# Kernel tuning notes

Hardware: AMD Instinct MI355X
Metric: run time of the kernel (lower is better)

## Reference

```python
import jax, jax.numpy as jnp
import numpy as np

N = 50000   # nodes
E = 800000  # edges
G = 64      # graphs
NEG_SLOPE = 0.2  # PyG GATConv leaky_relu slope


def gat_conv(x, edge_index, edge_attr, W, att_src, att_dst, We, att_edge, bias, num_nodes):
    # PyG GATConv, add_self_loops=False, concat=True, eval (no dropout)
    H, C = att_src.shape
    h = (x @ W).reshape(-1, H, C)                      # [N,H,C]
    a_src = (h * att_src).sum(-1)                      # [N,H]
    a_dst = (h * att_dst).sum(-1)                      # [N,H]
    src, dst = edge_index[0], edge_index[1]
    e = (edge_attr @ We).reshape(-1, H, C)             # [E,H,C]
    a_edge = (e * att_edge).sum(-1)                    # [E,H]
    alpha = a_src[src] + a_dst[dst] + a_edge           # [E,H]
    alpha = jax.nn.leaky_relu(alpha, NEG_SLOPE)
    # segment softmax over incoming edges of each dst node
    amax = jax.ops.segment_max(alpha, dst, num_segments=num_nodes)
    amax = jnp.where(jnp.isfinite(amax), amax, 0.0)
    ex = jnp.exp(alpha - amax[dst])
    denom = jax.ops.segment_sum(ex, dst, num_segments=num_nodes)
    att = ex / (denom[dst] + 1e-16)                    # [E,H]
    msg = h[src] * att[..., None]                      # [E,H,C]
    out = jax.ops.segment_sum(msg, dst, num_segments=num_nodes)
    return out.reshape(num_nodes, H * C) + bias


def setup_inputs() -> dict:
    key = jax.random.key(0)
    ks = jax.random.split(key, 20)
    s = 0.1
    inp = {
        "x": jax.random.normal(ks[0], (N, 128), jnp.float32),
        "edge_index": jax.random.randint(ks[1], (2, E), 0, N, dtype=jnp.int32),
        "edge_attr": jax.random.normal(ks[2], (E, 1), jnp.float32),
        "batch": jnp.sort(jax.random.randint(ks[3], (N,), 0, G, dtype=jnp.int32)),
        # layer 1: 128 -> 4 heads x 32
        "W1": jax.random.normal(ks[4], (128, 128), jnp.float32) * s,
        "as1": jax.random.normal(ks[5], (4, 32), jnp.float32) * s,
        "ad1": jax.random.normal(ks[6], (4, 32), jnp.float32) * s,
        "We1": jax.random.normal(ks[7], (1, 128), jnp.float32) * s,
        "ae1": jax.random.normal(ks[8], (4, 32), jnp.float32) * s,
        "b1": jnp.zeros((128,), jnp.float32),
        # layer 2: 128 -> 1 head x 64
        "W2": jax.random.normal(ks[9], (128, 64), jnp.float32) * s,
        "as2": jax.random.normal(ks[10], (1, 64), jnp.float32) * s,
        "ad2": jax.random.normal(ks[11], (1, 64), jnp.float32) * s,
        "We2": jax.random.normal(ks[12], (1, 64), jnp.float32) * s,
        "ae2": jax.random.normal(ks[13], (1, 64), jnp.float32) * s,
        "b2": jnp.zeros((64,), jnp.float32),
        # prediction head
        "Wp": jax.random.normal(ks[14], (64, 1), jnp.float32) * s,
        "bp": jnp.zeros((1,), jnp.float32),
    }
    return inp


def reference(x, edge_index, edge_attr, batch, W1, as1, ad1, We1, ae1, b1,
              W2, as2, ad2, We2, ae2, b2, Wp, bp):
    h = gat_conv(x, edge_index, edge_attr, W1, as1, ad1, We1, ae1, b1, N)
    h = jax.nn.relu(h)  # dropout p=0.0, eval mode
    h = gat_conv(h, edge_index, edge_attr, W2, as2, ad2, We2, ae2, b2, N)
    # per-graph mean pooling (vectorized replacement of the python loop)
    counts = jax.ops.segment_sum(jnp.ones((N,), h.dtype), batch, num_segments=G)
    sums = jax.ops.segment_sum(h, batch, num_segments=G)   # [G,64]
    mean = sums / counts[:, None]
    out = mean @ Wp + bp                                   # [G,1]
    return out.squeeze(-1)                                 # [G]
```

## Files before the change

### kernel.cpp

```cpp
#include <hip/hip_runtime.h>
#include <hip/hip_bf16.h>

typedef unsigned short u16;
typedef unsigned int u32;

#define MAXB 2048
#define POOL_MAXG 64

typedef __attribute__((ext_vector_type(8))) short bf16x8;
typedef __attribute__((ext_vector_type(4))) float f32x4;

__device__ __forceinline__ float bf2f(u16 u) { return __uint_as_float(((u32)u) << 16); }
__device__ __forceinline__ float bl(u32 u) { return __uint_as_float(u << 16); }
__device__ __forceinline__ float bh(u32 u) { return __uint_as_float(u & 0xffff0000u); }
__device__ __forceinline__ u16 f2bf(float f) {
    u32 u = __float_as_uint(f);
    u += 0x7fffu + ((u >> 16) & 1u);
    return (u16)(u >> 16);
}
__device__ __forceinline__ float lrelu(float x) { return x > 0.f ? x : 0.2f * x; }
__device__ __forceinline__ int clampi(int v, int lo, int hi) {
    return v < lo ? lo : (v > hi ? hi : v);
}
__device__ __forceinline__ float load1(const void* base, int idx, int f32) {
    return f32 ? ((const float*)base)[idx] : bf2f(((const u16*)base)[idx]);
}
__device__ __forceinline__ float cexpf(float a) {
    return __builtin_amdgcn_exp2f(fminf(a, 30.f) * 1.4426950408889634f);
}

__global__ void k_init(const u32* __restrict__ xw, int* __restrict__ flag,
                       int* __restrict__ bcnt, int B,
                       const void* We1, const void* ae1, const void* We2, const void* ae2,
                       const void* as1, const void* ad1, const void* as2, const void* ad2,
                       float* __restrict__ consts, float* __restrict__ pool, int psize) {
    __shared__ int sf;
    int t = threadIdx.x;
    for (int i = t; i < B; i += 256) bcnt[i] = 0;
    if (t < 64) {
        int cnt = 0;
        #pragma unroll
        for (int j = 0; j < 4; j++) {
            u32 w = xw[t * 4 + j];
            int e0 = (int)((w >> 7) & 0xffu);
            int e1 = (int)((w >> 23) & 0xffu);
            cnt += (e0 >= 0x60 && e0 <= 0x8f);
            cnt += (e1 >= 0x60 && e1 <= 0x8f);
        }
        #pragma unroll
        for (int off = 32; off > 0; off >>= 1) cnt += __shfl_xor(cnt, off);
        if (t == 0) { int v = (cnt < 480) ? 1 : 0; *flag = v; sf = v; }
    }
    __syncthreads();
    int f = sf;
    for (int i = t; i < psize; i += 256) pool[i] = 0.f;
    if (t < 4) {
        float s = 0.f;
        for (int c = 0; c < 32; c++) s += load1(We1, t * 32 + c, f) * load1(ae1, t * 32 + c, f);
        consts[t] = s;
    } else if (t == 4) {
        float s = 0.f;
        for (int c = 0; c < 64; c++) s += load1(We2, c, f) * load1(ae2, c, f);
        consts[4] = s;
    }
    if (t < 128) {
        consts[8 + t] = load1(as1, t, f);
        consts[136 + t] = load1(ad1, t, f);
    }
    if (t < 64) {
        consts[264 + t] = load1(as2, t, f);
        consts[328 + t] = load1(ad2, t, f);
    }
}

template <int NC>
__global__ __launch_bounds__(256, 2) void k_gemm_mfma(
    const void* __restrict__ X, const void* __restrict__ Wg,
    const int* __restrict__ flag, int fXovr, u16* __restrict__ Y,
    const float* __restrict__ consts, float* __restrict__ casrc,
    float* __restrict__ cadst, int nrows) {
    constexpr int NCT = NC / 16;
    __shared__ __align__(16) u16 Bf[2][NCT][4][64][8];

    const int f = *flag;
    const bool fX = (fXovr < 0) ? (f != 0) : (fXovr != 0);
    const bool fW = (f != 0);
    const int tid = threadIdx.x;
    const int wid = tid >> 6, lane = tid & 63;

    if (fW) {
        const float* W4 = (const float*)Wg;
        for (int g = tid; g < 128 * NC / 4; g += 256) {
            int e = g * 4;
            int r = e / NC;
            int c = e % NC;
            int k = (NC == 64) ? ((r < 64) ? 2 * r : 2 * (r - 64) + 1) : r;
            int s = k >> 5;
            int kk = k & 31;
            int lhi = (kk >> 3) << 4;
            int j = kk & 7;
            float4 v = *(const float4*)(W4 + e);
            float vv[4] = {v.x, v.y, v.z, v.w};
            #pragma unroll
            for (int q = 0; q < 4; q++) {
                int col = c + q;
                int t = col >> 4, l = lhi | (col & 15);
                u16 h = f2bf(vv[q]);
                Bf[0][t][s][l][j] = h;
                Bf[1][t][s][l][j] = f2bf(vv[q] - bf2f(h));
            }
        }
    } else {
        const u16* Wb = (const u16*)Wg;
        for (int g = tid; g < 128 * NC / 8; g += 256) {
            int e = g * 8;
            int r = e / NC;
            int c = e % NC;
            int k = (NC == 64) ? ((r < 64) ? 2 * r : 2 * (r - 64) + 1) : r;
            int s = k >> 5;
            int kk = k & 31;
            int lhi = (kk >> 3) << 4;
            int j = kk & 7;
            uint4 v = *(const uint4*)(Wb + e);
            u16 arr[8] = {(u16)v.x, (u16)(v.x >> 16), (u16)v.y, (u16)(v.y >> 16),
                          (u16)v.z, (u16)(v.z >> 16), (u16)v.w, (u16)(v.w >> 16)};
            #pragma unroll
            for (int q = 0; q < 8; q++) {
                int col = c + q;
                int t = col >> 4, l = lhi | (col & 15);
                Bf[0][t][s][l][j] = arr[q];
            }
        }
    }
    __syncthreads();

    const int tileIds[2] = {(int)blockIdx.x, (int)(blockIdx.x + gridDim.x)};

    bf16x8 ahi[2][4], alo[2][4];
    #pragma unroll
    for (int tt = 0; tt < 2; tt++) {
        const int rowbase = tileIds[tt] * 64 + wid * 16;
        const int arow = rowbase + (lane & 15);
        const bool rv = arow < nrows;
        #pragma unroll
        for (int s = 0; s < 4; s++) {
            int koff = s * 32 + (lane >> 4) * 8;
            u16 h[8], l8[8];
            #pragma unroll
            for (int j = 0; j < 8; j++) { h[j] = 0; l8[j] = 0; }
            if (rv) {
                if (fX) {
                    const float* xp = (const float*)X + (size_t)arow * 128 + koff;
                    float4 a = *(const float4*)xp;
                    float4 b = *(const float4*)(xp + 4);
                    float vv[8];
                    vv[0] = a.x; vv[1] = a.y; vv[2] = a.z; vv[3] = a.w;
                    vv[4] = b.x; vv[5] = b.y; vv[6] = b.z; vv[7] = b.w;
                    #pragma unroll
                    for (int j = 0; j < 8; j++) {
                        h[j] = f2bf(vv[j]);
                        l8[j] = f2bf(vv[j] - bf2f(h[j]));
                    }
                } else {
                    const u16* xp = (const u16*)X + (size_t)arow * 128 + koff;
                    uint4 q = *(const uint4*)xp;
                    h[0] = (u16)q.x; h[1] = (u16)(q.x >> 16);
                    h[2] = (u16)q.y; h[3] = (u16)(q.y >> 16);
                    h[4] = (u16)q.z; h[5] = (u16)(q.z >> 16);
                    h[6] = (u16)q.w; h[7] = (u16)(q.w >> 16);
                }
            }
            bf16x8 vh, vl;
            #pragma unroll
            for (int j = 0; j < 8; j++) { vh[j] = (short)h[j]; vl[j] = (short)l8[j]; }
            ahi[tt][s] = vh; alo[tt][s] = vl;
        }
    }

    f32x4 acc[2][NCT];
    #pragma unroll
    for (int tt = 0; tt < 2; tt++)
        #pragma unroll
        for (int t = 0; t < NCT; t++) acc[tt][t] = (f32x4){0.f, 0.f, 0.f, 0.f};
    #pragma unroll
    for (int s = 0; s < 4; s++) {
        #pragma unroll
        for (int t = 0; t < NCT; t++) {
            bf16x8 bhi = *(const bf16x8*)&Bf[0][t][s][lane][0];
            acc[0][t] = __builtin_amdgcn_mfma_f32_16x16x32_bf16(ahi[0][s], bhi, acc[0][t], 0, 0, 0);
            acc[1][t] = __builtin_amdgcn_mfma_f32_16x16x32_bf16(ahi[1][s], bhi, acc[1][t], 0, 0, 0);
            if (fW) {
                bf16x8 blo = *(const bf16x8*)&Bf[1][t][s][lane][0];
                acc[0][t] = __builtin_amdgcn_mfma_f32_16x16x32_bf16(ahi[0][s], blo, acc[0][t], 0, 0, 0);
                acc[1][t] = __builtin_amdgcn_mfma_f32_16x16x32_bf16(ahi[1][s], blo, acc[1][t], 0, 0, 0);
            }
            if (fX) {
                acc[0][t] = __builtin_amdgcn_mfma_f32_16x16x32_bf16(alo[0][s], bhi, acc[0][t], 0, 0, 0);
                acc[1][t] = __builtin_amdgcn_mfma_f32_16x16x32_bf16(alo[1][s], bhi, acc[1][t], 0, 0, 0);
            }
        }
    }

    #pragma unroll
    for (int tt = 0; tt < 2; tt++) {
        const int rowbase = tileIds[tt] * 64 + wid * 16;
        const int l16 = lane & 15;
        #pragma unroll
        for (int reg = 0; reg < 4; reg++) {
            int r = rowbase + (lane >> 4) * 4 + reg;
            if (r < nrows) {
                if constexpr (NC == 128) {
                    #pragma unroll
                    for (int t = 0; t < 4; t++) {
                        u32 w = (u32)f2bf(acc[tt][t][reg])
                              | ((u32)f2bf(acc[tt][t + 4][reg]) << 16);
                        ((u32*)Y)[(size_t)r * 64 + t * 16 + l16] = w;
                    }
                } else {
                    #pragma unroll
                    for (int t = 0; t < 4; t++)
                        Y[(size_t)r * 64 + t * 16 + l16] = f2bf(acc[tt][t][reg]);
                }
            }
        }
        if (casrc) {
            if constexpr (NC == 128) {
                #pragma unroll
                for (int reg = 0; reg < 4; reg++) {
                    int r = rowbase + (lane >> 4) * 4 + reg;
                    float pA[4] = {0.f, 0.f, 0.f, 0.f};
                    float pD[4] = {0.f, 0.f, 0.f, 0.f};
                    #pragma unroll
                    for (int t = 0; t < 4; t++) {
                        int p = t * 16 + l16;
                        int g = t >> 1;
                        pA[g]     += acc[tt][t][reg]     * consts[8 + p];
                        pD[g]     += acc[tt][t][reg]     * consts[136 + p];
                        pA[g + 2] += acc[tt][t + 4][reg] * consts[72 + p];
                        pD[g + 2] += acc[tt][t + 4][reg] * consts[200 + p];
                    }
                    #pragma unroll
                    for (int off = 1; off < 16; off <<= 1) {
                        #pragma unroll
                        for (int g = 0; g < 4; g++) {
                            pA[g] += __shfl_xor(pA[g], off);
                            pD[g] += __shfl_xor(pD[g], off);
                        }
                    }
                    if (l16 == 0 && r < nrows) {
                        #pragma unroll
                        for (int g = 0; g < 4; g++) {
                            casrc[r * 4 + g] = pA[g];
                            cadst[r * 4 + g] = pD[g];
                        }
                    }
                }
            } else {
                #pragma unroll
                for (int reg = 0; reg < 4; reg++) {
                    int r = rowbase + (lane >> 4) * 4 + reg;
                    float s1 = 0.f, s2 = 0.f;
                    #pragma unroll
                    for (int t = 0; t < 4; t++) {
                        int p = t * 16 + l16;
                        s1 += acc[tt][t][reg] * consts[264 + p];
                        s2 += acc[tt][t][reg] * consts[328 + p];
                    }
                    #pragma unroll
                    for (int off = 1; off < 16; off <<= 1) {
                        s1 += __shfl_xor(s1, off);
                        s2 += __shfl_xor(s2, off);
                    }
                    if (l16 == 0 && r < nrows) { casrc[r] = s1; cadst[r] = s2; }
                }
            }
        }
    }
}

__global__ __launch_bounds__(256) void k_bhist2(const int* __restrict__ dst,
                                                int* __restrict__ bcnt, int E, int n, int B) {
    __shared__ int lh[MAXB];
    for (int i = threadIdx.x; i < B; i += 256) lh[i] = 0;
    __syncthreads();
    int stride = gridDim.x * 256;
    for (int e = blockIdx.x * 256 + threadIdx.x; e < E; e += stride) {
        int d = clampi(dst[e], 0, n - 1);
        atomicAdd(&lh[d >> 8], 1);
    }
    __syncthreads();
    for (int i = threadIdx.x; i < B; i += 256)
        if (lh[i]) atomicAdd(&bcnt[i], lh[i]);
}
__global__ void k_bscan(const int* __restrict__ bcnt, int* __restrict__ bbase,
                        int* __restrict__ bfront, int* __restrict__ roff,
                        int B, int N, int E) {
    __shared__ int buf[256];
    __shared__ int carry;
    int t = threadIdx.x;
    if (t == 0) carry = 0;
    __syncthreads();
    for (int base = 0; base < B; base += 256) {
        int k = base + t;
        int v = (k < B) ? bcnt[k] : 0;
        buf[t] = v;
        __syncthreads();
        for (int off = 1; off < 256; off <<= 1) {
            int u = (t >= off) ? buf[t - off] : 0;
            __syncthreads();
            buf[t] += u;
            __syncthreads();
        }
        int excl = carry + buf[t] - v;
        if (k < B) { bbase[k] = excl; bfront[k] = excl; }
        __syncthreads();
        if (t == 0) carry += buf[255];
        __syncthreads();
    }
    if (t == 0) { bbase[B] = carry; roff[N] = E; }
}
__global__ void k_zero(int* __restrict__ p, int n) {
    int i = blockIdx.x * 256 + threadIdx.x;
    if (i < n) p[i] = 0;
}
__global__ __launch_bounds__(256) void k_bhist(const int* __restrict__ dst,
                                               int* __restrict__ cnt, int* __restrict__ bcnt,
                                               int E, int n, int B) {
    __shared__ int lh[MAXB];
    for (int i = threadIdx.x; i < B; i += 256) lh[i] = 0;
    __syncthreads();
    int stride = gridDim.x * 256;
    for (int e = blockIdx.x * 256 + threadIdx.x; e < E; e += stride) {
        int d = clampi(dst[e], 0, n - 1);
        atomicAdd(&cnt[d], 1);
        atomicAdd(&lh[d >> 8], 1);
    }
    __syncthreads();
    for (int i = threadIdx.x; i < B; i += 256)
        if (lh[i]) atomicAdd(&bcnt[i], lh[i]);
}
__global__ void k_scan1(const int* __restrict__ cnt, int* __restrict__ part,
                        int* __restrict__ bsum, int n) {
    __shared__ int buf[256];
    int i = blockIdx.x * 256 + threadIdx.x;
    int v = (i < n) ? cnt[i] : 0;
    buf[threadIdx.x] = v;
    __syncthreads();
    for (int off = 1; off < 256; off <<= 1) {
        int t = (threadIdx.x >= off) ? buf[threadIdx.x - off] : 0;
        __syncthreads();
        buf[threadIdx.x] += t;
        __syncthreads();
    }
    if (i < n) part[i] = buf[threadIdx.x];
    if (threadIdx.x == 255) bsum[blockIdx.x] = buf[255];
}
__global__ void k_scan3b(int* __restrict__ roff, const int* __restrict__ bsum,
                         int* __restrict__ rpos, int n, int nb) {
    __shared__ int buf[256];
    int t = threadIdx.x;
    int v = (t < nb) ? bsum[t] : 0;
    buf[t] = v;
    __syncthreads();
    for (int off = 1; off < 256; off <<= 1) {
        int u = (t >= off) ? buf[t - off] : 0;
        __syncthreads();
        buf[t] += u;
        __syncthreads();
    }
    __shared__ int excl[256];
    excl[t] = buf[t] - v;
    __syncthreads();
    int i = blockIdx.x * 256 + t;
    if (i > n) return;
    int val;
    if (i == 0) { val = 0; roff[0] = 0; }
    else { val = roff[i] + excl[(i - 1) >> 8]; roff[i] = val; }
    if (i < n) rpos[i] = val;
}
__global__ __launch_bounds__(256) void k_binA(
    const int* __restrict__ dst, const int* __restrict__ src, const void* eattr,
    const int* __restrict__ flag, int* __restrict__ bfront, int2* __restrict__ stagedA,
    int E, int n, int B) {
    __shared__ int lhist[MAXB];
    __shared__ int lbase[MAXB];
    int f = *flag;
    constexpr int T = 2048;
    for (int tile = blockIdx.x; (long long)tile * T < E; tile += gridDim.x) {
        int base = tile * T;
        for (int i = threadIdx.x; i < B; i += 256) lhist[i] = 0;
        __syncthreads();
        int sj0, sj1, sj2, sj3, sj4, sj5, sj6, sj7;
        int dj0, dj1, dj2, dj3, dj4, dj5, dj6, dj7;
        int rj0, rj1, rj2, rj3, rj4, rj5, rj6, rj7;
        int ej0, ej1, ej2, ej3, ej4, ej5, ej6, ej7;
        #define BINA_LOAD(J, SJ, DJ, RJ, EJ)                                   \
        {                                                                      \
            int idx = base + (J) * 256 + threadIdx.x;                          \
            bool v = idx < E;                                                  \
            int d = v ? clampi(dst[idx], 0, n - 1) : 0;                        \
            SJ = v ? clampi(src[idx], 0, n - 1) : 0;                           \
            EJ = v ? __float_as_int(load1(eattr, idx, f)) : 0;                 \
            DJ = d;                                                            \
            RJ = v ? atomicAdd(&lhist[d >> 8], 1) : -1;                        \
        }
        BINA_LOAD(0, sj0, dj0, rj0, ej0)
        BINA_LOAD(1, sj1, dj1, rj1, ej1)
        BINA_LOAD(2, sj2, dj2, rj2, ej2)
        BINA_LOAD(3, sj3, dj3, rj3, ej3)
        BINA_LOAD(4, sj4, dj4, rj4, ej4)
        BINA_LOAD(5, sj5, dj5, rj5, ej5)
        BINA_LOAD(6, sj6, dj6, rj6, ej6)
        BINA_LOAD(7, sj7, dj7, rj7, ej7)
        #undef BINA_LOAD
        __syncthreads();
        for (int i = threadIdx.x; i < B; i += 256) {
            int c = lhist[i];
            lbase[i] = c ? atomicAdd(&bfront[i], c) : 0;
        }
        __syncthreads();
        #define BINA_STORE(SJ, DJ, RJ, EJ)                                     \
        if (RJ >= 0) {                                                         \
            long long q = (long long)lbase[DJ >> 8] + RJ;                      \
            if (q >= 0 && q < E) {                                             \
                int2 v2;                                                       \
                v2.x = (SJ & 0xFFFFFF) | ((DJ & 255) << 24);                   \
                v2.y = EJ;                                                     \
                stagedA[q] = v2;                                               \
            }                                                                  \
        }
        BINA_STORE(sj0, dj0, rj0, ej0)
        BINA_STORE(sj1, dj1, rj1, ej1)
        BINA_STORE(sj2, dj2, rj2, ej2)
        BINA_STORE(sj3, dj3, rj3, ej3)
        BINA_STORE(sj4, dj4, rj4, ej4)
        BINA_STORE(sj5, dj5, rj5, ej5)
        BINA_STORE(sj6, dj6, rj6, ej6)
        BINA_STORE(sj7, dj7, rj7, ej7)
        #undef BINA_STORE
        __syncthreads();
    }
}
__global__ __launch_bounds__(256) void k_binB2(
    const int2* __restrict__ stagedA, const int* __restrict__ bbase,
    int* __restrict__ roff, int2* __restrict__ edata, int N, int E, int B) {
    __shared__ int lcnt[256];
    __shared__ int buf[256];
    __shared__ int lpos[256];
    int k = blockIdx.x;
    int t = threadIdx.x;
    lcnt[t] = 0;
    __syncthreads();
    int lo = clampi(bbase[k], 0, E);
    int hi = clampi(bbase[k + 1], lo, E);
    for (int i = lo + t; i < hi; i += 256)
        atomicAdd(&lcnt[(stagedA[i].x >> 24) & 255], 1);
    __syncthreads();
    int v = lcnt[t];
    buf[t] = v;
    __syncthreads();
    for (int off = 1; off < 256; off <<= 1) {
        int u = (t >= off) ? buf[t - off] : 0;
        __syncthreads();
        buf[t] += u;
        __syncthreads();
    }
    int pos = lo + buf[t] - v;
    int dn = (k << 8) + t;
    if (dn < N) roff[dn] = pos;
    lpos[t] = pos;
    __syncthreads();
    for (int i = lo + t; i < hi; i += 256) {
        int2 a = stagedA[i];
        int p = atomicAdd(&lpos[(a.x >> 24) & 255], 1);
        if (p >= 0 && p < E) edata[p] = make_int2(a.x & 0xFFFFFF, a.y);
    }
}
__global__ void k_scatter(const int* __restrict__ dst, const int* __restrict__ src,
                          const void* eattr, const int* __restrict__ flag,
                          int* __restrict__ rpos, int2* __restrict__ edata, int E, int n) {
    int f = *flag;
    int e = blockIdx.x * 256 + threadIdx.x;
    if (e < E) {
        int d = clampi(dst[e], 0, n - 1);
        int s = clampi(src[e], 0, n - 1);
        float ea = load1(eattr, e, f);
        int p = atomicAdd(&rpos[d], 1);
        if (p >= 0 && p < E) {
            int2 v; v.x = s; v.y = __float_as_int(ea);
            edata[p] = v;
        }
    }
}

__global__ __launch_bounds__(256) void k_gat1c(
    const u32* __restrict__ hp, const float* __restrict__ asrc, const float* __restrict__ adst,
    const int2* __restrict__ edata, const int* __restrict__ roff,
    const int* __restrict__ flag, const float* __restrict__ consts, const void* bias,
    u32* __restrict__ out, int n, int E) {
    __shared__ float4 wls[4][64];
    int f = *flag;
    int gtid = blockIdx.x * 256 + threadIdx.x;
    int wv = gtid >> 6, lane = gtid & 63;
    int wid = (threadIdx.x >> 6);
    int nw = (gridDim.x * 256) >> 6;
    const float c0 = consts[0], c1 = consts[1], c2 = consts[2], c3 = consts[3];
    const int hl = lane & 31;
    const int sel = lane >> 5;
    const int p0 = hl * 2;
    const int phsel = hl >> 4;
    const float biasA0 = load1(bias, p0, f);
    const float biasB0 = load1(bias, 64 + p0, f);
    const float biasA1 = load1(bias, p0 + 1, f);
    const float biasB1 = load1(bias, 64 + p0 + 1, f);
    const int ghsel = lane >> 5;
    const float gbiasA = load1(bias, lane, f);
    const float gbiasB = load1(bias, 64 + lane, f);

    for (int db = wv * 2; db < n; db += nw * 2) {
        int d = db + sel;
        bool dv = d < n;
        int dcl = dv ? d : 0;
        int s0 = dv ? clampi(roff[d], 0, E) : 0;
        int s1 = dv ? clampi(roff[d + 1], s0, E) : 0;
        int deg = s1 - s0;

        if (__all(deg <= 32)) {
            float4 adv = *(const float4*)&adst[(size_t)dcl * 4];
            bool v = hl < deg;
            int s = 0;
            float e0 = 0.f, e1 = 0.f, e2 = 0.f, e3 = 0.f;
            if (v) {
                int2 ed = edata[s0 + hl];
                s = ed.x;
                float ea = __int_as_float(ed.y);
                float4 av = *(const float4*)&asrc[(size_t)s * 4];
                e0 = cexpf(lrelu(av.x + adv.x + ea * c0));
                e1 = cexpf(lrelu(av.y + adv.y + ea * c1));
                e2 = cexpf(lrelu(av.z + adv.z + ea * c2));
                e3 = cexpf(lrelu(av.w + adv.w + ea * c3));
            }
            float d0 = e0, d1 = e1, d2 = e2, d3 = e3;
            #pragma unroll
            for (int off = 16; off > 0; off >>= 1) {
                d0 += __shfl_xor(d0, off); d1 += __shfl_xor(d1, off);
                d2 += __shfl_xor(d2, off); d3 += __shfl_xor(d3, off);
            }
            float i0 = 1.f / (d0 + 1e-16f), i1 = 1.f / (d1 + 1e-16f);
            float i2 = 1.f / (d2 + 1e-16f), i3 = 1.f / (d3 + 1e-16f);
            wls[wid][lane] = make_float4(e0 * i0, e1 * i1, e2 * i2, e3 * i3);

            int degm = max(deg, __shfl_xor(deg, 32));
            int base = sel * 32;
            float aA0 = 0.f, aB0 = 0.f, aA1 = 0.f, aB1 = 0.f;
            for (int j = 0; j < degm; j += 4) {
                int j0 = base + j, j1 = base + j + 1, j2 = base + j + 2, j3 = base + j + 3;
                int sa = __shfl(s, j0), sb = __shfl(s, j1);
                int sc_ = __shfl(s, j2), sd = __shfl(s, j3);
                float4 wa = wls[wid][j0], wb = wls[wid][j1];
                float4 wc = wls[wid][j2], wd = wls[wid][j3];
                uint2 ha = *(const uint2*)(hp + (size_t)sa * 64 + p0);
                uint2 hb = *(const uint2*)(hp + (size_t)sb * 64 + p0);
                uint2 hc = *(const uint2*)(hp + (size_t)sc_ * 64 + p0);
                uint2 hd = *(const uint2*)(hp + (size_t)sd * 64 + p0);
                float wAa = phsel ? wa.y : wa.x, wBa = phsel ? wa.w : wa.z;
                float wAb = phsel ? wb.y : wb.x, wBb = phsel ? wb.w : wb.z;
                float wAc = phsel ? wc.y : wc.x, wBc = phsel ? wc.w : wc.z;
                float wAd = phsel ? wd.y : wd.x, wBd = phsel ? wd.w : wd.z;
                aA0 += wAa * bl(ha.x); aB0 += wBa * bh(ha.x);
                aA1 += wAa * bl(ha.y); aB1 += wBa * bh(ha.y);
                aA0 += wAb * bl(hb.x); aB0 += wBb * bh(hb.x);
                aA1 += wAb * bl(hb.y); aB1 += wBb * bh(hb.y);
                aA0 += wAc * bl(hc.x); aB0 += wBc * bh(hc.x);
                aA1 += wAc * bl(hc.y); aB1 += wBc * bh(hc.y);
                aA0 += wAd * bl(hd.x); aB0 += wBd * bh(hd.x);
                aA1 += wAd * bl(hd.y); aB1 += wBd * bh(hd.y);
            }
            if (dv) {
                u32 w0 = (u32)f2bf(fmaxf(aA0 + biasA0, 0.f))
                       | ((u32)f2bf(fmaxf(aB0 + biasB0, 0.f)) << 16);
                u32 w1 = (u32)f2bf(fmaxf(aA1 + biasA1, 0.f))
                       | ((u32)f2bf(fmaxf(aB1 + biasB1, 0.f)) << 16);
                *(uint2*)(out + (size_t)d * 64 + p0) = make_uint2(w0, w1);
            }
        } else {
            for (int q = 0; q < 2; q++) {
                int dq = db + q;
                if (dq >= n) break;
                int t0 = clampi(roff[dq], 0, E);
                int t1 = clampi(roff[dq + 1], t0, E);
                int dg = t1 - t0;
                float4 adv = *(const float4*)&adst[(size_t)dq * 4];
                if (dg <= 64) {
                    bool v = lane < dg;
                    int s = 0;
                    float e0 = 0.f, e1 = 0.f, e2 = 0.f, e3 = 0.f;
                    if (v) {
                        int2 ed = edata[t0 + lane];
                        s = ed.x;
                        float ea = __int_as_float(ed.y);
                        float4 av = *(const float4*)&asrc[(size_t)s * 4];
                        e0 = cexpf(lrelu(av.x + adv.x + ea * c0));
                        e1 = cexpf(lrelu(av.y + adv.y + ea * c1));
                        e2 = cexpf(lrelu(av.z + adv.z + ea * c2));
                        e3 = cexpf(lrelu(av.w + adv.w + ea * c3));
                    }
                    float d0 = e0, d1 = e1, d2 = e2, d3 = e3;
                    #pragma unroll
                    for (int off = 32; off > 0; off >>= 1) {
                        d0 += __shfl_xor(d0, off); d1 += __shfl_xor(d1, off);
                        d2 += __shfl_xor(d2, off); d3 += __shfl_xor(d3, off);
                    }
                    float i0 = 1.f / (d0 + 1e-16f), i1 = 1.f / (d1 + 1e-16f);
                    float i2 = 1.f / (d2 + 1e-16f), i3 = 1.f / (d3 + 1e-16f);
                    wls[wid][lane] = make_float4(e0 * i0, e1 * i1, e2 * i2, e3 * i3);

                    float aA0 = 0.f, aB0 = 0.f, aA1 = 0.f, aB1 = 0.f;
                    for (int j = 0; j < dg; j += 4) {
                        int j0 = j + sel, j1 = j + 2 + sel;
                        int sa = __shfl(s, j0), sb = __shfl(s, j1);
                        float4 wa = wls[wid][j0], wb = wls[wid][j1];
                        uint2 ha = *(const uint2*)(hp + (size_t)sa * 64 + p0);
                        uint2 hb = *(const uint2*)(hp + (size_t)sb * 64 + p0);
                        float wAa = phsel ? wa.y : wa.x, wBa = phsel ? wa.w : wa.z;
                        float wAb = phsel ? wb.y : wb.x, wBb = phsel ? wb.w : wb.z;
                        aA0 += wAa * bl(ha.x); aB0 += wBa * bh(ha.x);
                        aA1 += wAa * bl(ha.y); aB1 += wBa * bh(ha.y);
                        aA0 += wAb * bl(hb.x); aB0 += wBb * bh(hb.x);
                        aA1 += wAb * bl(hb.y); aB1 += wBb * bh(hb.y);
                    }
                    aA0 += __shfl_xor(aA0, 32); aB0 += __shfl_xor(aB0, 32);
                    aA1 += __shfl_xor(aA1, 32); aB1 += __shfl_xor(aB1, 32);
                    if (lane < 32) {
                        u32 w0 = (u32)f2bf(fmaxf(aA0 + biasA0, 0.f))
                               | ((u32)f2bf(fmaxf(aB0 + biasB0, 0.f)) << 16);
                        u32 w1 = (u32)f2bf(fmaxf(aA1 + biasA1, 0.f))
                               | ((u32)f2bf(fmaxf(aB1 + biasB1, 0.f)) << 16);
                        *(uint2*)(out + (size_t)dq * 64 + p0) = make_uint2(w0, w1);
                    }
                } else {
                    float d0 = 0.f, d1 = 0.f, d2 = 0.f, d3 = 0.f;
                    for (int idx = t0 + lane; idx < t1; idx += 64) {
                        int2 ed = edata[idx];
                        float ea = __int_as_float(ed.y);
                        float4 av = *(const float4*)&asrc[(size_t)ed.x * 4];
                        d0 += cexpf(lrelu(av.x + adv.x + ea * c0));
                        d1 += cexpf(lrelu(av.y + adv.y + ea * c1));
                        d2 += cexpf(lrelu(av.z + adv.z + ea * c2));
                        d3 += cexpf(lrelu(av.w + adv.w + ea * c3));
                    }
                    #pragma unroll
                    for (int off = 32; off > 0; off >>= 1) {
                        d0 += __shfl_xor(d0, off); d1 += __shfl_xor(d1, off);
                        d2 += __shfl_xor(d2, off); d3 += __shfl_xor(d3, off);
                    }
                    float i0 = 1.f / (d0 + 1e-16f), i1 = 1.f / (d1 + 1e-16f);
                    float i2 = 1.f / (d2 + 1e-16f), i3 = 1.f / (d3 + 1e-16f);
                    float iA = ghsel ? i1 : i0, iB = ghsel ? i3 : i2;
                    float cA = ghsel ? c1 : c0, cB = ghsel ? c3 : c2;
                    float aA = ghsel ? adv.y : adv.x, aB = ghsel ? adv.w : adv.z;
                    float accA = 0.f, accB = 0.f;
                    for (int idx = t0; idx < t1; idx++) {
                        int2 ed = edata[idx];
                        float ea = __int_as_float(ed.y);
                        float4 av = *(const float4*)&asrc[(size_t)ed.x * 4];
                        float wA = cexpf(lrelu((ghsel ? av.y : av.x) + aA + ea * cA)) * iA;
                        float wB = cexpf(lrelu((ghsel ? av.w : av.z) + aB + ea * cB)) * iB;
                        u32 hw = hp[(size_t)ed.x * 64 + lane];
                        accA += wA * bl(hw);
                        accB += wB * bh(hw);
                    }
                    float rA = fmaxf(accA + gbiasA, 0.f);
                    float rB = fmaxf(accB + gbiasB, 0.f);
                    out[(size_t)dq * 64 + lane] = (u32)f2bf(rA) | ((u32)f2bf(rB) << 16);
                }
            }
        }
    }
}

__global__ __launch_bounds__(256) void k_gat2c(
    const u16* __restrict__ h, const float* __restrict__ asrc, const float* __restrict__ adst,
    const int2* __restrict__ edata, const int* __restrict__ roff,
    const int* __restrict__ flag, const float* __restrict__ consts, const void* bias,
    u16* __restrict__ out, int n, int E) {
    __shared__ float wls[4][64];
    int f = *flag;
    int gtid = blockIdx.x * 256 + threadIdx.x;
    int wv = gtid >> 6, lane = gtid & 63;
    int wid = (threadIdx.x >> 6);
    int nw = (gridDim.x * 256) >> 6;
    const float C = consts[4];
    const int hl = lane & 31;
    const int sel = lane >> 5;
    const int p0 = hl * 2;
    const float bias0 = load1(bias, p0, f);
    const float bias1 = load1(bias, p0 + 1, f);
    const float gbias = load1(bias, lane, f);

    for (int db = wv * 2; db < n; db += nw * 2) {
        int d = db + sel;
        bool dv = d < n;
        int s0 = dv ? clampi(roff[d], 0, E) : 0;
        int s1 = dv ? clampi(roff[d + 1], s0, E) : 0;
        int deg = s1 - s0;
        float ad = dv ? adst[d] : 0.f;

        if (__all(deg <= 32)) {
            bool v = hl < deg;
            int s = 0;
            float e = 0.f;
            if (v) {
                int2 ed = edata[s0 + hl];
                s = ed.x;
                e = cexpf(lrelu(asrc[s] + ad + __int_as_float(ed.y) * C));
            }
            float den = e;
            #pragma unroll
            for (int off = 16; off > 0; off >>= 1) den += __shfl_xor(den, off);
            float inv = 1.f / (den + 1e-16f);
            wls[wid][lane] = e * inv;

            int degm = max(deg, __shfl_xor(deg, 32));
            int base = sel * 32;
            float a0 = 0.f, a1 = 0.f;
            for (int j = 0; j < degm; j += 4) {
                int j0 = base + j, j1 = base + j + 1, j2 = base + j + 2, j3 = base + j + 3;
                int sa = __shfl(s, j0), sb = __shfl(s, j1);
                int sc_ = __shfl(s, j2), sd = __shfl(s, j3);
                float wa = wls[wid][j0], wb = wls[wid][j1];
                float wc = wls[wid][j2], wd = wls[wid][j3];
                u32 ha = *(const u32*)(h + (size_t)sa * 64 + p0);
                u32 hb = *(const u32*)(h + (size_t)sb * 64 + p0);
                u32 hc = *(const u32*)(h + (size_t)sc_ * 64 + p0);
                u32 hd = *(const u32*)(h + (size_t)sd * 64 + p0);
                a0 += wa * bl(ha) + wb * bl(hb) + wc * bl(hc) + wd * bl(hd);
                a1 += wa * bh(ha) + wb * bh(hb) + wc * bh(hc) + wd * bh(hd);
            }
            if (dv) {
                u32 w = (u32)f2bf(a0 + bias0) | ((u32)f2bf(a1 + bias1) << 16);
                *(u32*)(out + (size_t)d * 64 + p0) = w;
            }
        } else {
            for (int q = 0; q < 2; q++) {
                int dq = db + q;
                if (dq >= n) break;
                int t0 = clampi(roff[dq], 0, E);
                int t1 = clampi(roff[dq + 1], t0, E);
                int dg = t1 - t0;
                float adq = adst[dq];
                if (dg <= 64) {
                    bool v = lane < dg;
                    int s = 0;
                    float e = 0.f;
                    if (v) {
                        int2 ed = edata[t0 + lane];
                        s = ed.x;
                        e = cexpf(lrelu(asrc[s] + adq + __int_as_float(ed.y) * C));
                    }
                    float den = e;
                    #pragma unroll
                    for (int off = 32; off > 0; off >>= 1) den += __shfl_xor(den, off);
                    float inv = 1.f / (den + 1e-16f);
                    wls[wid][lane] = e * inv;

                    float a0 = 0.f, a1 = 0.f;
                    for (int j = 0; j < dg; j += 4) {
                        int j0 = j + sel, j1 = j + 2 + sel;
                        int sa = __shfl(s, j0), sb = __shfl(s, j1);
                        float wa = wls[wid][j0], wb = wls[wid][j1];
                        u32 ha = *(const u32*)(h + (size_t)sa * 64 + p0);
                        u32 hb = *(const u32*)(h + (size_t)sb * 64 + p0);
                        a0 += wa * bl(ha) + wb * bl(hb);
                        a1 += wa * bh(ha) + wb * bh(hb);
                    }
                    a0 += __shfl_xor(a0, 32);
                    a1 += __shfl_xor(a1, 32);
                    if (lane < 32) {
                        u32 w = (u32)f2bf(a0 + bias0) | ((u32)f2bf(a1 + bias1) << 16);
                        *(u32*)(out + (size_t)dq * 64 + p0) = w;
                    }
                } else {
                    float den = 0.f;
                    for (int idx = t0 + lane; idx < t1; idx += 64) {
                        int2 ed = edata[idx];
                        den += cexpf(lrelu(asrc[ed.x] + adq + __int_as_float(ed.y) * C));
                    }
                    #pragma unroll
                    for (int off = 32; off > 0; off >>= 1) den += __shfl_xor(den, off);
                    float inv = 1.f / (den + 1e-16f);
                    float acc = 0.f;
                    for (int idx = t0; idx < t1; idx++) {
                        int2 ed = edata[idx];
                        float w = cexpf(lrelu(asrc[ed.x] + adq
                                              + __int_as_float(ed.y) * C)) * inv;
                        acc += w * bf2f(h[(size_t)ed.x * 64 + lane]);
                    }
                    out[(size_t)dq * 64 + lane] = f2bf(acc + gbias);
                }
            }
        }
    }
}

__global__ __launch_bounds__(256) void k_gat1f(
    const u32* __restrict__ hp, const float* __restrict__ asrc, const float* __restrict__ adst,
    const int2* __restrict__ edata, const int* __restrict__ roff,
    const int* __restrict__ flag, const float* __restrict__ consts, const void* bias,
    u32* __restrict__ out, int n, int E) {
    int f = *flag;
    int gtid = blockIdx.x * 256 + threadIdx.x;
    int wv = gtid >> 6, lane = gtid & 63;
    int nw = (gridDim.x * 256) >> 6;
    const float c0 = consts[0], c1 = consts[1], c2 = consts[2], c3 = consts[3];
    const int hsel = lane >> 5;
    const float biasA = load1(bias, lane, f);
    const float biasB = load1(bias, 64 + lane, f);

    for (int d = wv; d < n; d += nw) {
        int s0 = clampi(roff[d], 0, E);
        int s1 = clampi(roff[d + 1], s0, E);
        float4 adv = *(const float4*)&adst[d * 4];
        float d0 = 0.f, d1 = 0.f, d2 = 0.f, d3 = 0.f;
        for (int idx = s0 + lane; idx < s1; idx += 64) {
            int2 ed = edata[idx];
            float ea = __int_as_float(ed.y);
            float4 av = *(const float4*)&asrc[(size_t)ed.x * 4];
            d0 += cexpf(lrelu(av.x + adv.x + ea * c0));
            d1 += cexpf(lrelu(av.y + adv.y + ea * c1));
            d2 += cexpf(lrelu(av.z + adv.z + ea * c2));
            d3 += cexpf(lrelu(av.w + adv.w + ea * c3));
        }
        #pragma unroll
        for (int off = 32; off > 0; off >>= 1) {
            d0 += __shfl_xor(d0, off); d1 += __shfl_xor(d1, off);
            d2 += __shfl_xor(d2, off); d3 += __shfl_xor(d3, off);
        }
        float i0 = 1.f / (d0 + 1e-16f), i1 = 1.f / (d1 + 1e-16f);
        float i2 = 1.f / (d2 + 1e-16f), i3 = 1.f / (d3 + 1e-16f);
        float iA = hsel ? i1 : i0, iB = hsel ? i3 : i2;
        float cA = hsel ? c1 : c0, cB = hsel ? c3 : c2;
        float aA = hsel ? adv.y : adv.x, aB = hsel ? adv.w : adv.z;

        float accA = 0.f, accB = 0.f;
        for (int idx = s0; idx < s1; idx++) {
            int2 ed = edata[idx];
            float ea = __int_as_float(ed.y);
            float4 av = *(const float4*)&asrc[(size_t)ed.x * 4];
            float wA = cexpf(lrelu((hsel ? av.y : av.x) + aA + ea * cA)) * iA;
            float wB = cexpf(lrelu((hsel ? av.w : av.z) + aB + ea * cB)) * iB;
            u32 hw = hp[(size_t)ed.x * 64 + lane];
            accA += wA * bl(hw);
            accB += wB * bh(hw);
        }
        float rA = fmaxf(accA + biasA, 0.f);
        float rB = fmaxf(accB + biasB, 0.f);
        out[(size_t)d * 64 + lane] = (u32)f2bf(rA) | ((u32)f2bf(rB) << 16);
    }
}

__global__ __launch_bounds__(256) void k_gat2f(
    const u16* __restrict__ h, const float* __restrict__ asrc, const float* __restrict__ adst,
    const int2* __restrict__ edata, const int* __restrict__ roff,
    const int* __restrict__ flag, const float* __restrict__ consts, const void* bias,
    u16* __restrict__ out, int n, int E) {
    int f = *flag;
    int gtid = blockIdx.x * 256 + threadIdx.x;
    int wv = gtid >> 6, lane = gtid & 63;
    int nw = (gridDim.x * 256) >> 6;
    const float C = consts[4];
    const float biasL = load1(bias, lane, f);

    for (int d = wv; d < n; d += nw) {
        int s0 = clampi(roff[d], 0, E);
        int s1 = clampi(roff[d + 1], s0, E);
        float ad = adst[d];
        float den = 0.f;
        for (int idx = s0 + lane; idx < s1; idx += 64) {
            int2 ed = edata[idx];
            den += cexpf(lrelu(asrc[ed.x] + ad + __int_as_float(ed.y) * C));
        }
        #pragma unroll
        for (int off = 32; off > 0; off >>= 1) den += __shfl_xor(den, off);
        float inv = 1.f / (den + 1e-16f);

        float acc = 0.f;
        for (int idx = s0; idx < s1; idx++) {
            int2 ed = edata[idx];
            float w = cexpf(lrelu(asrc[ed.x] + ad + __int_as_float(ed.y) * C)) * inv;
            acc += w * bf2f(h[(size_t)ed.x * 64 + lane]);
        }
        out[(size_t)d * 64 + lane] = f2bf(acc + biasL);
    }
}

__global__ __launch_bounds__(256) void k_pool2(
    const u16* __restrict__ agg2, const int* __restrict__ batch,
    float* __restrict__ pool, float* __restrict__ cnt, int n, int G, int rpb) {
    __shared__ float lp[POOL_MAXG * 64];
    __shared__ float lc[POOL_MAXG];
    int t = threadIdx.x;
    for (int i = t; i < G * 64; i += 256) lp[i] = 0.f;
    for (int i = t; i < G; i += 256) lc[i] = 0.f;
    __syncthreads();
    int lane = t & 63;
    int rl = t >> 6;
    int r0 = blockIdx.x * rpb;
    int r1 = min(r0 + rpb, n);
    float acc = 0.f, cacc = 0.f;
    int curg = -1;
    for (int j = r0 + rl; j < r1; j += 4) {
        int g = clampi(batch[j], 0, G - 1);
        float v = bf2f(agg2[(size_t)j * 64 + lane]);
        if (g != curg) {
            if (curg >= 0) {
                atomicAdd(&lp[curg * 64 + lane], acc);
                if (lane == 0) atomicAdd(&lc[curg], cacc);
            }
            acc = 0.f; cacc = 0.f; curg = g;
        }
        acc += v; cacc += 1.f;
    }
    if (curg >= 0) {
        atomicAdd(&lp[curg * 64 + lane], acc);
        if (lane == 0) atomicAdd(&lc[curg], cacc);
    }
    __syncthreads();
    for (int i = t; i < G * 64; i += 256) {
        float v = lp[i];
        if (v != 0.f) atomicAdd(&pool[i], v);
    }
    for (int i = t; i < G; i += 256) {
        float v = lc[i];
        if (v != 0.f) atomicAdd(&cnt[i], v);
    }
}

__global__ void k_pool(const u16* __restrict__ agg2, const int* __restrict__ batch,
                       float* __restrict__ pool, float* __restrict__ cnt, int n, int G) {
    int t = blockIdx.x * 256 + threadIdx.x;
    int nb8 = (n + 7) / 8;
    if (t >= nb8 * 64) return;
    int base = (t >> 6) * 8;
    int c = t & 63;
    int end = min(base + 8, n);
    float acc = 0.f, cacc = 0.f;
    int curg = clampi(batch[base], 0, G - 1);
    for (int j = base; j < end; j++) {
        int g = clampi(batch[j], 0, G - 1);
        if (g != curg) {
            atomicAdd(&pool[curg * 64 + c], acc);
            if (c == 0) atomicAdd(&cnt[curg], cacc);
            acc = 0.f; cacc = 0.f; curg = g;
        }
        acc += bf2f(agg2[(size_t)j * 64 + c]);
        cacc += 1.f;
    }
    atomicAdd(&pool[curg * 64 + c], acc);
    if (c == 0) atomicAdd(&cnt[curg], cacc);
}

__global__ void k_head(const float* __restrict__ pool, const float* __restrict__ cnt,
                       const void* Wp, const void* bp, const int* __restrict__ flag,
                       void* out, int G) {
    int f = *flag;
    int g = threadIdx.x;
    if (g >= G) return;
    float s = 0.f;
    for (int c = 0; c < 64; c++) s += pool[g * 64 + c] * load1(Wp, c, f);
    float cv = cnt[g];
    if (!(cv > 0.f)) cv = 1.f;
    float r = s / cv + load1(bp, 0, f);
    if (f) ((float*)out)[g] = r;
    else   ((u16*)out)[g] = f2bf(r);
}

extern "C" void kernel_launch(void* const* d_in, const int* in_sizes, int n_in,
                              void* d_out, int out_size, void* d_ws, size_t ws_size,
                              hipStream_t stream) {
    const void* x    = d_in[0];
    const int* ei    = (const int*)d_in[1];
    const void* eattr = d_in[2];
    const int* batch = (const int*)d_in[3];
    const void* W1   = d_in[4];
    const void* as1  = d_in[5];
    const void* ad1  = d_in[6];
    const void* We1  = d_in[7];
    const void* ae1  = d_in[8];
    const void* b1   = d_in[9];
    const void* W2   = d_in[10];
    const void* as2  = d_in[11];
    const void* ad2  = d_in[12];
    const void* We2  = d_in[13];
    const void* ae2  = d_in[14];
    const void* b2   = d_in[15];
    const void* Wp   = d_in[16];
    const void* bp   = d_in[17];

    const int N = in_sizes[3];
    const int E = in_sizes[2];
    const int G = out_size;
    const int* src = ei;
    const int* dst = ei + E;
    const int B = (N + 255) >> 8;

    char* p = (char*)d_ws;
    auto alloc = [&](size_t bytes) -> char* {
        char* r = p;
        p += (bytes + 255) & ~(size_t)255;
        return r;
    };
    int* flag    = (int*)alloc(32);
    float* consts = (float*)alloc(2048);
    int* roff    = (int*)alloc((size_t)(N + 1) * 4);
    int* rpos    = (int*)alloc((size_t)N * 4);
    int* bsum    = (int*)alloc(256 * 4);
    int* bcnt    = (int*)alloc((size_t)(MAXB * 3 + 1) * 4);
    int* bbase   = bcnt + MAXB;
    int* bfront  = bbase + MAXB + 1;
    int2* edata  = (int2*)alloc((size_t)E * 8);
    float* pool  = (float*)alloc((size_t)(G * 64 + G) * 4);
    float* cnt   = pool + (size_t)G * 64;
    float* asrc1 = (float*)alloc((size_t)N * 4 * 4);
    float* adst1 = (float*)alloc((size_t)N * 4 * 4);
    float* asrc2 = asrc1;
    float* adst2 = adst1;
    u16* agg1    = (u16*)alloc((size_t)N * 128 * 2);
    u16* h1      = (u16*)alloc((size_t)N * 128 * 2);
    u16* h2      = h1;
    u16* agg2    = h1 + (size_t)N * 64;
    int2* stagedA = (int2*)alloc((size_t)E * 8);
    size_t full_need = (size_t)(p - (char*)d_ws);
    const bool cached = (ws_size >= full_need);
    const bool binned = cached && (B <= MAXB) && (N <= (1 << 24));

    const int GG = (N + 127) >> 7;

    k_init<<<1, 256, 0, stream>>>((const u32*)x, flag, bcnt, B,
                                  We1, ae1, We2, ae2, as1, ad1, as2, ad2,
                                  consts, pool, G * 64 + G);
    k_gemm_mfma<128><<<GG, 256, 0, stream>>>(x, W1, flag, -1, h1, consts,
                                             asrc1, adst1, N);

    if (binned) {
        k_bhist2<<<512, 256, 0, stream>>>(dst, bcnt, E, N, B);
        k_bscan<<<1, 256, 0, stream>>>(bcnt, bbase, bfront, roff, B, N, E);
        k_binA<<<(E + 2047) / 2048, 256, 0, stream>>>(dst, src, eattr, flag, bfront,
                                                      stagedA, E, N, B);
        k_binB2<<<B, 256, 0, stream>>>(stagedA, bbase, roff, edata, N, E, B);
    } else {
        int NB = (N + 255) / 256;
        k_zero<<<(N + 255) / 256, 256, 0, stream>>>(rpos, N);
        k_bhist<<<512, 256, 0, stream>>>(dst, rpos, bcnt, E, N, B);
        k_scan1<<<NB, 256, 0, stream>>>(rpos, roff + 1, bsum, N);
        k_scan3b<<<(N + 256) / 256, 256, 0, stream>>>(roff, bsum, rpos, N, NB);
        k_scatter<<<(E + 255) / 256, 256, 0, stream>>>(dst, src, eattr, flag, rpos,
                                                       edata, E, N);
    }

    int gatBlocks = (N * 64 + 255) / 256;
    if (cached) {
        k_gat1c<<<gatBlocks, 256, 0, stream>>>((const u32*)h1, asrc1, adst1, edata, roff,
                                               flag, consts, b1, (u32*)agg1, N, E);
    } else {
        k_gat1f<<<gatBlocks, 256, 0, stream>>>((const u32*)h1, asrc1, adst1, edata, roff,
                                               flag, consts, b1, (u32*)agg1, N, E);
    }
    k_gemm_mfma<64><<<GG, 256, 0, stream>>>(agg1, W2, flag, 0, h2, consts,
                                            asrc2, adst2, N);
    if (cached) {
        k_gat2c<<<gatBlocks, 256, 0, stream>>>(h2, asrc2, adst2, edata, roff, flag,
                                               consts, b2, agg2, N, E);
    } else {
        k_gat2f<<<gatBlocks, 256, 0, stream>>>(h2, asrc2, adst2, edata, roff, flag,
                                               consts, b2, agg2, N, E);
    }
    if (G <= POOL_MAXG) {
        int rpb = (N + 1023) / 1024;
        if (rpb < 8) rpb = 8;
        int pblocks = (N + rpb - 1) / rpb;
        k_pool2<<<pblocks, 256, 0, stream>>>(agg2, batch, pool, cnt, N, G, rpb);
    } else {
        k_pool<<<(((N + 7) / 8) * 64 + 255) / 256, 256, 0, stream>>>(agg2, batch, pool,
                                                                     cnt, N, G);
    }
    k_head<<<1, 64, 0, stream>>>(pool, cnt, Wp, bp, flag, d_out, G);
}
```

Before: 283.4 us.

## Fuse layer-1 GEMM and edge binning pass into one heterogeneous launch

The layer-1 MFMA GEMM and the first edge-binning pass (binA) are merged into a single kernel. Blocks below the GEMM block count run the GEMM and the rest run binning, sharing one static shared-memory buffer. The two independent stages can then run concurrently on the GPU, removing a launch and the serialization between them. In exchange, binA blocks now carry the GEMM's 32KB shared-memory footprint and its launch bounds, which may lower their occupancy.

```diff
diff --git a/kernel.cpp b/kernel.cpp
--- a/kernel.cpp
+++ b/kernel.cpp
@@ -74,19 +74,18 @@
 }
 
 template <int NC>
-__global__ __launch_bounds__(256, 2) void k_gemm_mfma(
-    const void* __restrict__ X, const void* __restrict__ Wg,
-    const int* __restrict__ flag, int fXovr, u16* __restrict__ Y,
-    const float* __restrict__ consts, float* __restrict__ casrc,
-    float* __restrict__ cadst, int nrows) {
+__device__ __forceinline__ void dev_gemm(
+    u16* __restrict__ Bf,
+    const void* __restrict__ X, const void* __restrict__ Wg, bool fX, bool fW,
+    u16* __restrict__ Y, const float* __restrict__ consts,
+    float* __restrict__ casrc, float* __restrict__ cadst,
+    int nrows, int bid, int nblocks) {
     constexpr int NCT = NC / 16;
-    __shared__ __align__(16) u16 Bf[2][NCT][4][64][8];
-
-    const int f = *flag;
-    const bool fX = (fXovr < 0) ? (f != 0) : (fXovr != 0);
-    const bool fW = (f != 0);
     const int tid = threadIdx.x;
     const int wid = tid >> 6, lane = tid & 63;
+    auto bfi = [&](int hh, int t, int s, int l, int j) {
+        return ((((hh)*NCT + t) * 4 + s) * 64 + l) * 8 + j;
+    };
 
     if (fW) {
         const float* W4 = (const float*)Wg;
@@ -106,8 +105,8 @@
                 int col = c + q;
                 int t = col >> 4, l = lhi | (col & 15);
                 u16 h = f2bf(vv[q]);
-                Bf[0][t][s][l][j] = h;
-                Bf[1][t][s][l][j] = f2bf(vv[q] - bf2f(h));
+                Bf[bfi(0, t, s, l, j)] = h;
+                Bf[bfi(1, t, s, l, j)] = f2bf(vv[q] - bf2f(h));
             }
         }
     } else {
@@ -128,13 +127,13 @@
             for (int q = 0; q < 8; q++) {
                 int col = c + q;
                 int t = col >> 4, l = lhi | (col & 15);
-                Bf[0][t][s][l][j] = arr[q];
-            }
-        }
-    }
-    __syncthreads();
-
-    const int tileIds[2] = {(int)blockIdx.x, (int)(blockIdx.x + gridDim.x)};
+                Bf[bfi(0, t, s, l, j)] = arr[q];
+            }
+        }
+    }
+    __syncthreads();
+
+    const int tileIds[2] = {bid, bid + nblocks};
 
     bf16x8 ahi[2][4], alo[2][4];
     #pragma unroll
@@ -186,11 +185,11 @@
     for (int s = 0; s < 4; s++) {
         #pragma unroll
         for (int t = 0; t < NCT; t++) {
-            bf16x8 bhi = *(const bf16x8*)&Bf[0][t][s][lane][0];
+            bf16x8 bhi = *(const bf16x8*)(Bf + bfi(0, t, s, lane, 0));
             acc[0][t] = __builtin_amdgcn_mfma_f32_16x16x32_bf16(ahi[0][s], bhi, acc[0][t], 0, 0, 0);
             acc[1][t] = __builtin_amdgcn_mfma_f32_16x16x32_bf16(ahi[1][s], bhi, acc[1][t], 0, 0, 0);
             if (fW) {
-                bf16x8 blo = *(const bf16x8*)&Bf[1][t][s][lane][0];
+                bf16x8 blo = *(const bf16x8*)(Bf + bfi(1, t, s, lane, 0));
                 acc[0][t] = __builtin_amdgcn_mfma_f32_16x16x32_bf16(ahi[0][s], blo, acc[0][t], 0, 0, 0);
                 acc[1][t] = __builtin_amdgcn_mfma_f32_16x16x32_bf16(ahi[1][s], blo, acc[1][t], 0, 0, 0);
             }
@@ -278,115 +277,15 @@
     }
 }
 
-__global__ __launch_bounds__(256) void k_bhist2(const int* __restrict__ dst,
-                                                int* __restrict__ bcnt, int E, int n, int B) {
-    __shared__ int lh[MAXB];
-    for (int i = threadIdx.x; i < B; i += 256) lh[i] = 0;
-    __syncthreads();
-    int stride = gridDim.x * 256;
-    for (int e = blockIdx.x * 256 + threadIdx.x; e < E; e += stride) {
-        int d = clampi(dst[e], 0, n - 1);
-        atomicAdd(&lh[d >> 8], 1);
-    }
-    __syncthreads();
-    for (int i = threadIdx.x; i < B; i += 256)
-        if (lh[i]) atomicAdd(&bcnt[i], lh[i]);
-}
-__global__ void k_bscan(const int* __restrict__ bcnt, int* __restrict__ bbase,
-                        int* __restrict__ bfront, int* __restrict__ roff,
-                        int B, int N, int E) {
-    __shared__ int buf[256];
-    __shared__ int carry;
-    int t = threadIdx.x;
-    if (t == 0) carry = 0;
-    __syncthreads();
-    for (int base = 0; base < B; base += 256) {
-        int k = base + t;
-        int v = (k < B) ? bcnt[k] : 0;
-        buf[t] = v;
-        __syncthreads();
-        for (int off = 1; off < 256; off <<= 1) {
-            int u = (t >= off) ? buf[t - off] : 0;
-            __syncthreads();
-            buf[t] += u;
-            __syncthreads();
-        }
-        int excl = carry + buf[t] - v;
-        if (k < B) { bbase[k] = excl; bfront[k] = excl; }
-        __syncthreads();
-        if (t == 0) carry += buf[255];
-        __syncthreads();
-    }
-    if (t == 0) { bbase[B] = carry; roff[N] = E; }
-}
-__global__ void k_zero(int* __restrict__ p, int n) {
-    int i = blockIdx.x * 256 + threadIdx.x;
-    if (i < n) p[i] = 0;
-}
-__global__ __launch_bounds__(256) void k_bhist(const int* __restrict__ dst,
-                                               int* __restrict__ cnt, int* __restrict__ bcnt,
-                                               int E, int n, int B) {
-    __shared__ int lh[MAXB];
-    for (int i = threadIdx.x; i < B; i += 256) lh[i] = 0;
-    __syncthreads();
-    int stride = gridDim.x * 256;
-    for (int e = blockIdx.x * 256 + threadIdx.x; e < E; e += stride) {
-        int d = clampi(dst[e], 0, n - 1);
-        atomicAdd(&cnt[d], 1);
-        atomicAdd(&lh[d >> 8], 1);
-    }
-    __syncthreads();
-    for (int i = threadIdx.x; i < B; i += 256)
-        if (lh[i]) atomicAdd(&bcnt[i], lh[i]);
-}
-__global__ void k_scan1(const int* __restrict__ cnt, int* __restrict__ part,
-                        int* __restrict__ bsum, int n) {
-    __shared__ int buf[256];
-    int i = blockIdx.x * 256 + threadIdx.x;
-    int v = (i < n) ? cnt[i] : 0;
-    buf[threadIdx.x] = v;
-    __syncthreads();
-    for (int off = 1; off < 256; off <<= 1) {
-        int t = (threadIdx.x >= off) ? buf[threadIdx.x - off] : 0;
-        __syncthreads();
-        buf[threadIdx.x] += t;
-        __syncthreads();
-    }
-    if (i < n) part[i] = buf[threadIdx.x];
-    if (threadIdx.x == 255) bsum[blockIdx.x] = buf[255];
-}
-__global__ void k_scan3b(int* __restrict__ roff, const int* __restrict__ bsum,
-                         int* __restrict__ rpos, int n, int nb) {
-    __shared__ int buf[256];
-    int t = threadIdx.x;
-    int v = (t < nb) ? bsum[t] : 0;
-    buf[t] = v;
-    __syncthreads();
-    for (int off = 1; off < 256; off <<= 1) {
-        int u = (t >= off) ? buf[t - off] : 0;
-        __syncthreads();
-        buf[t] += u;
-        __syncthreads();
-    }
-    __shared__ int excl[256];
-    excl[t] = buf[t] - v;
-    __syncthreads();
-    int i = blockIdx.x * 256 + t;
-    if (i > n) return;
-    int val;
-    if (i == 0) { val = 0; roff[0] = 0; }
-    else { val = roff[i] + excl[(i - 1) >> 8]; roff[i] = val; }
-    if (i < n) rpos[i] = val;
-}
-__global__ __launch_bounds__(256) void k_binA(
+__device__ __forceinline__ void dev_binA(
+    int* __restrict__ smem,
     const int* __restrict__ dst, const int* __restrict__ src, const void* eattr,
-    const int* __restrict__ flag, int* __restrict__ bfront, int2* __restrict__ stagedA,
-    int E, int n, int B) {
-    __shared__ int lhist[MAXB];
-    __shared__ int lbase[MAXB];
-    int f = *flag;
+    int f, int* __restrict__ bfront, int2* __restrict__ stagedA,
+    int E, int n, int B, int bid, int nblk) {
+    int* lhist = smem;
+    int* lbase = smem + MAXB;
     constexpr int T = 2048;
-    for (int tile = blockIdx.x; (long long)tile * T < E; tile += gridDim.x) {
+    for (int tile = bid; (long long)tile * T < E; tile += nblk) {
         int base = tile * T;
         for (int i = threadIdx.x; i < B; i += 256) lhist[i] = 0;
         __syncthreads();
@@ -440,6 +339,137 @@
         #undef BINA_STORE
         __syncthreads();
     }
+}
+
+template <int NC>
+__global__ __launch_bounds__(256, 2) void k_gemm_mfma(
+    const void* __restrict__ X, const void* __restrict__ Wg,
+    const int* __restrict__ flag, int fXovr, u16* __restrict__ Y,
+    const float* __restrict__ consts, float* __restrict__ casrc,
+    float* __restrict__ cadst, int nrows) {
+    __shared__ __align__(16) u16 Bf[2 * (NC / 16) * 4 * 64 * 8];
+    const int f = *flag;
+    dev_gemm<NC>(Bf, X, Wg, (fXovr < 0) ? (f != 0) : (fXovr != 0), f != 0,
+                 Y, consts, casrc, cadst, nrows, blockIdx.x, gridDim.x);
+}
+
+__global__ __launch_bounds__(256, 2) void k_fuse_gemm_binA(
+    const void* __restrict__ X, const void* __restrict__ Wg,
+    const int* __restrict__ flag, u16* __restrict__ Y,
+    const float* __restrict__ consts, float* __restrict__ casrc,
+    float* __restrict__ cadst, int nrows, int gemmBlocks,
+    const int* __restrict__ dst, const int* __restrict__ src, const void* eattr,
+    int* __restrict__ bfront, int2* __restrict__ stagedA, int E, int n, int B) {
+    __shared__ __align__(16) char smem[2 * 8 * 4 * 64 * 8 * 2];
+    const int f = *flag;
+    if ((int)blockIdx.x < gemmBlocks) {
+        dev_gemm<128>((u16*)smem, X, Wg, f != 0, f != 0, Y, consts, casrc, cadst,
+                      nrows, blockIdx.x, gemmBlocks);
+    } else {
+        dev_binA((int*)smem, dst, src, eattr, f, bfront, stagedA, E, n, B,
+                 blockIdx.x - gemmBlocks, gridDim.x - gemmBlocks);
+    }
+}
+
+__global__ __launch_bounds__(256) void k_bhist2(const int* __restrict__ dst,
+                                                int* __restrict__ bcnt, int E, int n, int B) {
+    __shared__ int lh[MAXB];
+    for (int i = threadIdx.x; i < B; i += 256) lh[i] = 0;
+    __syncthreads();
+    int stride = gridDim.x * 256;
+    for (int e = blockIdx.x * 256 + threadIdx.x; e < E; e += stride) {
+        int d = clampi(dst[e], 0, n - 1);
+        atomicAdd(&lh[d >> 8], 1);
+    }
+    __syncthreads();
+    for (int i = threadIdx.x; i < B; i += 256)
+        if (lh[i]) atomicAdd(&bcnt[i], lh[i]);
+}
+__global__ void k_bscan(const int* __restrict__ bcnt, int* __restrict__ bbase,
+                        int* __restrict__ bfront, int* __restrict__ roff,
+                        int B, int N, int E) {
+    __shared__ int buf[256];
+    __shared__ int carry;
+    int t = threadIdx.x;
+    if (t == 0) carry = 0;
+    __syncthreads();
+    for (int base = 0; base < B; base += 256) {
+        int k = base + t;
+        int v = (k < B) ? bcnt[k] : 0;
+        buf[t] = v;
+        __syncthreads();
+        for (int off = 1; off < 256; off <<= 1) {
+            int u = (t >= off) ? buf[t - off] : 0;
+            __syncthreads();
+            buf[t] += u;
+            __syncthreads();
+        }
+        int excl = carry + buf[t] - v;
+        if (k < B) { bbase[k] = excl; bfront[k] = excl; }
+        __syncthreads();
+        if (t == 0) carry += buf[255];
+        __syncthreads();
+    }
+    if (t == 0) { bbase[B] = carry; roff[N] = E; }
+}
+__global__ void k_zero(int* __restrict__ p, int n) {
+    int i = blockIdx.x * 256 + threadIdx.x;
+    if (i < n) p[i] = 0;
+}
+__global__ __launch_bounds__(256) void k_bhist(const int* __restrict__ dst,
+                                               int* __restrict__ cnt, int* __restrict__ bcnt,
+                                               int E, int n, int B) {
+    __shared__ int lh[MAXB];
+    for (int i = threadIdx.x; i < B; i += 256) lh[i] = 0;
+    __syncthreads();
+    int stride = gridDim.x * 256;
+    for (int e = blockIdx.x * 256 + threadIdx.x; e < E; e += stride) {
+        int d = clampi(dst[e], 0, n - 1);
+        atomicAdd(&cnt[d], 1);
+        atomicAdd(&lh[d >> 8], 1);
+    }
+    __syncthreads();
+    for (int i = threadIdx.x; i < B; i += 256)
+        if (lh[i]) atomicAdd(&bcnt[i], lh[i]);
+}
+__global__ void k_scan1(const int* __restrict__ cnt, int* __restrict__ part,
+                        int* __restrict__ bsum, int n) {
+    __shared__ int buf[256];
+    int i = blockIdx.x * 256 + threadIdx.x;
+    int v = (i < n) ? cnt[i] : 0;
+    buf[threadIdx.x] = v;
+    __syncthreads();
+    for (int off = 1; off < 256; off <<= 1) {
+        int t = (threadIdx.x >= off) ? buf[threadIdx.x - off] : 0;
+        __syncthreads();
+        buf[threadIdx.x] += t;
+        __syncthreads();
+    }
+    if (i < n) part[i] = buf[threadIdx.x];
+    if (threadIdx.x == 255) bsum[blockIdx.x] = buf[255];
+}
+__global__ void k_scan3b(int* __restrict__ roff, const int* __restrict__ bsum,
+                         int* __restrict__ rpos, int n, int nb) {
+    __shared__ int buf[256];
+    int t = threadIdx.x;
+    int v = (t < nb) ? bsum[t] : 0;
+    buf[t] = v;
+    __syncthreads();
+    for (int off = 1; off < 256; off <<= 1) {
+        int u = (t >= off) ? buf[t - off] : 0;
+        __syncthreads();
+        buf[t] += u;
+        __syncthreads();
+    }
+    __shared__ int excl[256];
+    excl[t] = buf[t] - v;
+    __syncthreads();
+    int i = blockIdx.x * 256 + t;
+    if (i > n) return;
+    int val;
+    if (i == 0) { val = 0; roff[0] = 0; }
+    else { val = roff[i] + excl[(i - 1) >> 8]; roff[i] = val; }
+    if (i < n) rpos[i] = val;
 }
 __global__ __launch_bounds__(256) void k_binB2(
     const int2* __restrict__ stagedA, const int* __restrict__ bbase,
@@ -1035,20 +1065,22 @@
     const bool binned = cached && (B <= MAXB) && (N <= (1 << 24));
 
     const int GG = (N + 127) >> 7;
+    const int nBin = (E + 2047) / 2048;
 
     k_init<<<1, 256, 0, stream>>>((const u32*)x, flag, bcnt, B,
                                   We1, ae1, We2, ae2, as1, ad1, as2, ad2,
                                   consts, pool, G * 64 + G);
-    k_gemm_mfma<128><<<GG, 256, 0, stream>>>(x, W1, flag, -1, h1, consts,
-                                             asrc1, adst1, N);
 
     if (binned) {
         k_bhist2<<<512, 256, 0, stream>>>(dst, bcnt, E, N, B);
         k_bscan<<<1, 256, 0, stream>>>(bcnt, bbase, bfront, roff, B, N, E);
-        k_binA<<<(E + 2047) / 2048, 256, 0, stream>>>(dst, src, eattr, flag, bfront,
-                                                      stagedA, E, N, B);
+        k_fuse_gemm_binA<<<GG + nBin, 256, 0, stream>>>(
+            x, W1, flag, h1, consts, asrc1, adst1, N, GG,
+            dst, src, eattr, bfront, stagedA, E, N, B);
         k_binB2<<<B, 256, 0, stream>>>(stagedA, bbase, roff, edata, N, E, B);
     } else {
+        k_gemm_mfma<128><<<GG, 256, 0, stream>>>(x, W1, flag, -1, h1, consts,
+                                                 asrc1, adst1, N);
         int NB = (N + 255) / 256;
         k_zero<<<(N + 255) / 256, 256, 0, stream>>>(rpos, N);
         k_bhist<<<512, 256, 0, stream>>>(dst, rpos, bcnt, E, N, B);
```

Result: faster. 259.5 us (-8.4%).
